# Performance work log

Measured on AMD Instinct MI355X. Metric: run time of the kernel, lower is better.

## Reference

```python
import jax, jax.numpy as jnp
import numpy as np

N, M, FEAT, POS, D, MSG, NCLS = 64, 32, 256, 6, 262, 128, 7


def setup_inputs() -> dict:
    key = jax.random.key(0)
    ks = jax.random.split(key, 12)
    s = 0.05
    p = lambda k, shape: jax.random.normal(k, shape, jnp.float32) * s
    return {
        "nodes_feature": jax.random.normal(ks[0], (N, M, FEAT), jnp.float32),
        "pos": jax.random.normal(ks[1], (N, M, POS), jnp.float32),
        "num_rec": jax.random.randint(ks[2], (N,), 1, M + 1),
        "link_w1": p(ks[3], (D, 2 * D)),
        "link_b1": jnp.zeros((D,), jnp.float32),
        "link_w2": p(ks[4], (D,)),
        "link_b2": jnp.zeros((), jnp.float32),
        "msg_w": p(ks[5], (MSG, D)),
        "msg_b": jnp.zeros((MSG,), jnp.float32),
        "gru_w_ih": p(ks[6], (3 * D, MSG)),
        "gru_w_hh": p(ks[7], (3 * D, D)),
        "gru_b_ih": jnp.zeros((3 * D,), jnp.float32),
        "gru_b_hh": jnp.zeros((3 * D,), jnp.float32),
        "ro_w1": p(ks[8], (MSG, D)),
        "ro_b1": jnp.zeros((MSG,), jnp.float32),
        "ro_w2": p(ks[9], (NCLS, MSG)),
        "ro_b2": jnp.zeros((NCLS,), jnp.float32),
    }


def reference(nodes_feature, pos, num_rec, link_w1, link_b1, link_w2, link_b2,
              msg_w, msg_b, gru_w_ih, gru_w_hh, gru_b_ih, gru_b_hh,
              ro_w1, ro_b1, ro_w2, ro_b2):
    # node_feat = [resnet_feat, pos]  -> (N, M, 262)
    nf = jnp.concatenate([nodes_feature, pos], axis=-1)
    n, m, d = nf.shape
    valid = jnp.arange(m)[None, :] < num_rec[:, None]          # (N, M)
    pair = valid[:, :, None] & valid[:, None, :]               # (N, M, M)

    # edge_feat[b,:,i,j] = concat(nf[b,i], nf[b,j]); zero for invalid pairs
    ef = jnp.concatenate([
        jnp.broadcast_to(nf[:, :, None, :], (n, m, m, d)),
        jnp.broadcast_to(nf[:, None, :, :], (n, m, m, d)),
    ], axis=-1) * pair[..., None].astype(nf.dtype)             # (N, M, M, 2D)

    # 1x1 convs == per-pair MLP
    hlink = jax.nn.relu(jnp.einsum('bnwc,dc->bnwd', ef, link_w1) + link_b1)
    attmat = jax.nn.sigmoid(jnp.einsum('bnwd,d->bnw', hlink, link_w2) + link_b2)

    # messages are only summed over valid sender nodes w
    att_m = attmat * valid[:, None, :].astype(attmat.dtype)    # (N, M, M)

    def gru_step(x, h):
        # PyTorch GRU cell: gates order (r, z, n)
        gx = x @ gru_w_ih.T + gru_b_ih
        gh = h @ gru_w_hh.T + gru_b_hh
        xr, xz, xn = jnp.split(gx, 3, axis=-1)
        hr, hz, hn = jnp.split(gh, 3, axis=-1)
        r = jax.nn.sigmoid(xr + hr)
        z = jax.nn.sigmoid(xz + hz)
        c = jnp.tanh(xn + r * hn)
        return (1.0 - z) * c + z * h

    vmask = valid[..., None].astype(nf.dtype)
    h_state = nf                                               # pass 0 input state
    for _ in range(2):                                         # two message-passing rounds
        msg = h_state @ msg_w.T + msg_b                        # (N, M, 128)
        m_v = jnp.einsum('bnw,bwk->bnk', att_m, msg)           # attention-weighted sum
        h_state = gru_step(m_v, h_state) * vmask               # invalid nodes stay zero

    pred = (jax.nn.relu(h_state @ ro_w1.T + ro_b1) @ ro_w2.T + ro_b2) * vmask
    return pred, attmat
```

## Files before the change

### kernel.cpp

```cpp
#include <hip/hip_runtime.h>
#include <math.h>

#define N_G   64
#define M_N   32
#define FEAT  256
#define POSD  6
#define D     262
#define MSG   128
#define NCLS  7

#define KA_S  424
#define KHW   288
#define KFULL 416
#define PSTR  320

#define S_PROJ (528*288)
#define S_MSG  (128*288)
#define S_RZ   (544*416)
#define S_XN   (272*128)
#define S_HN   (272*288)
#define S_RO   (128*288)
#define S_RO2  (16*128)

#define O_WPROJ 0u
#define O_WMSG  76032u
#define O_WRZ   94464u
#define O_WXN   207616u
#define O_WHN   225024u
#define O_WRO   264192u
#define O_WRO2  282624u
#define O_GB    283648u

typedef __attribute__((ext_vector_type(8))) short short8;
typedef __attribute__((ext_vector_type(4))) short short4v;
typedef __attribute__((ext_vector_type(4))) float floatx4;

#define MFMA __builtin_amdgcn_mfma_f32_16x16x32_bf16

__device__ __forceinline__ short f2bf(float f) {
    union { float f; unsigned u; } v; v.f = f;
    unsigned r = v.u + 0x7FFF + ((v.u >> 16) & 1);
    return (short)(r >> 16);
}
__device__ __forceinline__ float bf2f(short s) {
    union { float f; unsigned u; } v;
    v.u = ((unsigned)(unsigned short)s) << 16;
    return v.f;
}
__device__ __forceinline__ float sigf(float x) {
    return __builtin_amdgcn_rcpf(1.f + __expf(-x));
}
__device__ __forceinline__ float tanh_fast(float x) {
    float e = __expf(-2.f * fabsf(x));
    float t = (1.f - e) * __builtin_amdgcn_rcpf(1.f + e);
    return copysignf(t, x);
}

__global__ __launch_bounds__(256) void prep_kernel(
    const float* __restrict__ w1, const float* __restrict__ msg_w,
    const float* __restrict__ w_ih, const float* __restrict__ w_hh,
    const float* __restrict__ ro_w1, const float* __restrict__ ro_w2,
    const float* __restrict__ b_ih, const float* __restrict__ b_hh,
    float* __restrict__ ws)
{
    short* wproj = (short*)(ws + O_WPROJ);
    short* wmsg  = (short*)(ws + O_WMSG);
    short* wrz   = (short*)(ws + O_WRZ);
    short* wxn   = (short*)(ws + O_WXN);
    short* whn   = (short*)(ws + O_WHN);
    short* wro   = (short*)(ws + O_WRO);
    short* wro2  = (short*)(ws + O_WRO2);
    float* gb    = ws + O_GB;

    int row = blockIdx.x * 4 + (threadIdx.x >> 6);
    const int lane = threadIdx.x & 63;
    if (row >= 1892) return;

    if (row < 528) {
        const int n = row;
        short* out = wproj + n * 288;
        const float* src = (n < D) ? (w1 + n * 524) : (w1 + (n - D) * 524 + D);
        for (int k = lane; k < 288; k += 64) {
            float v = (k < D && n < 524) ? src[k] : 0.f;
            out[k] = f2bf(v);
        }
        return;
    }
    row -= 528;
    if (row < 128) {
        const int n = row;
        short* out = wmsg + n * 288;
        const float* src = msg_w + n * D;
        for (int k = lane; k < 288; k += 64)
            out[k] = f2bf(k < D ? src[k] : 0.f);
        return;
    }
    row -= 128;
    if (row < 544) {
        const int g = row;
        const int gi = (g < 272) ? 0 : 1;
        const int d = g - gi * 272;
        short* out = wrz + g * 416;
        if (d < D) {
            const int r = gi * D + d;
            const float* sih = w_ih + r * MSG;
            const float* shh = w_hh + r * D - 128;
            for (int k = lane; k < 416; k += 64) {
                float v;
                if (k < 128)            v = sih[k];
                else if (k < 128 + D)   v = shh[k];
                else                    v = 0.f;
                out[k] = f2bf(v);
            }
        } else {
            for (int k = lane; k < 416; k += 64) out[k] = 0;
        }
        return;
    }
    row -= 544;
    if (row < 272) {
        const int d = row;
        short* out = wxn + d * 128;
        const float* src = w_ih + (2 * D + d) * MSG;
        for (int k = lane; k < 128; k += 64)
            out[k] = f2bf(d < D ? src[k] : 0.f);
        return;
    }
    row -= 272;
    if (row < 272) {
        const int d = row;
        short* out = whn + d * 288;
        const float* src = w_hh + (2 * D + d) * D;
        for (int k = lane; k < 288; k += 64)
            out[k] = f2bf((d < D && k < D) ? src[k] : 0.f);
        return;
    }
    row -= 272;
    if (row < 128) {
        const int n = row;
        short* out = wro + n * 288;
        const float* src = ro_w1 + n * D;
        for (int k = lane; k < 288; k += 64)
            out[k] = f2bf(k < D ? src[k] : 0.f);
        return;
    }
    row -= 128;
    if (row < 16) {
        const int n = row;
        short* out = wro2 + n * 128;
        const float* src = ro_w2 + n * MSG;
        for (int k = lane; k < 128; k += 64)
            out[k] = f2bf(n < NCLS ? src[k] : 0.f);
        return;
    }
    row -= 16;
    {
        const int seg = row;
        float* out = gb + seg * 272;
        for (int d = lane; d < 272; d += 64) {
            float v = 0.f;
            if (d < D) {
                if (seg == 0)      v = b_ih[d] + b_hh[d];
                else if (seg == 1) v = b_ih[D + d] + b_hh[D + d];
                else if (seg == 2) v = b_ih[2 * D + d];
                else               v = b_hh[2 * D + d];
            }
            out[d] = v;
        }
    }
}

__global__ __launch_bounds__(512, 2) void fused_kernel(
    const float* __restrict__ nodes, const float* __restrict__ pos,
    const int* __restrict__ nrec_g,
    const float* __restrict__ b1g, const float* __restrict__ w2g,
    const float* __restrict__ b2g, const float* __restrict__ msg_bg,
    const float* __restrict__ ro_b1g, const float* __restrict__ ro_b2g,
    const float* __restrict__ ws,
    float* __restrict__ att_out, float* __restrict__ pred)
{
    const short* Wproj = (const short*)(ws + O_WPROJ);
    const short* Wmsg  = (const short*)(ws + O_WMSG);
    const short* Wrz   = (const short*)(ws + O_WRZ);
    const short* Wxn   = (const short*)(ws + O_WXN);
    const short* Whn   = (const short*)(ws + O_WHN);
    const short* Wro   = (const short*)(ws + O_WRO);
    const short* Wro2  = (const short*)(ws + O_WRO2);
    const float* gb    = ws + O_GB;

    __shared__ __align__(16) short bufA[32 * KA_S];
    __shared__ __align__(16) short bufB[32 * KA_S];
    __shared__ __align__(16) short paL[32 * PSTR];
    __shared__ __align__(16) short pbL[32 * PSTR];
    __shared__ __align__(16) short attL[32 * 40];
    __shared__ __align__(16) short msgT[128 * 40];
    __shared__ __align__(16) short hidL[32 * 136];
    __shared__ __align__(16) float b1L[PSTR], w2L[PSTR];

    const int b = blockIdx.x;
    const int tid = threadIdx.x;
    const int wave = tid >> 6, lane = tid & 63;
    const int quad = lane >> 4, lrow = lane & 15;

    floatx4 prm[10];
    {
        const floatx4* pb = (const floatx4*)(ws + O_WRZ);
        const int base = wave * 64 + lane;
#pragma unroll
        for (int p = 0; p < 10; ++p)
            prm[p] = pb[(p * 512 + base) * 8];
    }
    short8 wvA[9];
    {
        const short* bw = Wproj + (wave * 16 + lrow) * KHW + quad * 8;
#pragma unroll
        for (int kk = 0; kk < 9; ++kk) wvA[kk] = *(const short8*)(bw + kk * 32);
    }

    const int nr = nrec_g[b];

    for (int idx = tid; idx < 32 * 64; idx += 512) {
        int w = idx >> 6, c4 = idx & 63;
        floatx4 v = *(const floatx4*)(nodes + ((size_t)(b * 32 + w)) * FEAT + c4 * 4);
        short4v s; s[0] = f2bf(v[0]); s[1] = f2bf(v[1]); s[2] = f2bf(v[2]); s[3] = f2bf(v[3]);
        *(short4v*)(bufA + w * KA_S + 128 + c4 * 4) = s;
    }
    for (int idx = tid; idx < 32 * POSD; idx += 512) {
        int w = idx / POSD, c = idx % POSD;
        bufA[w * KA_S + 128 + FEAT + c] = f2bf(pos[((size_t)(b * 32 + w)) * POSD + c]);
    }
    for (int idx = tid; idx < 32 * 34; idx += 512) {
        int w = idx / 34, c = idx % 34;
        bufA[w * KA_S + 390 + c] = 0;
        bufB[w * KA_S + 390 + c] = 0;
    }
    for (int idx = tid; idx < 32 * (PSTR - D); idx += 512) {
        int w = idx / (PSTR - D), c = idx % (PSTR - D);
        paL[w * PSTR + D + c] = 0;
        pbL[w * PSTR + D + c] = 0;
    }
    for (int d = tid; d < PSTR; d += 512) {
        b1L[d] = (d < D) ? b1g[d] : 0.f;
        w2L[d] = (d < D) ? w2g[d] : 0.f;
    }
#pragma unroll
    for (int p = 0; p < 10; ++p) asm volatile("" :: "v"(prm[p]));
    __syncthreads();

    {
        auto store_proj = [&](int s, floatx4 acc0, floatx4 acc1) {
            int col = s * 16 + lrow;
#pragma unroll
            for (int rr = 0; rr < 4; ++rr) {
                int r0 = quad * 4 + rr;
                if (col < D) {
                    paL[r0 * PSTR + col] = f2bf(acc0[rr]);
                    paL[(r0 + 16) * PSTR + col] = f2bf(acc1[rr]);
                } else if (col < 2 * D) {
                    pbL[r0 * PSTR + (col - D)] = f2bf(acc0[rr]);
                    pbL[(r0 + 16) * PSTR + (col - D)] = f2bf(acc1[rr]);
                }
            }
        };
        auto store_msg = [&](int s, floatx4 acc0, floatx4 acc1) {
            int col = (s - 33) * 16 + lrow;
            float bias = msg_bg[col];
#pragma unroll
            for (int rr = 0; rr < 4; ++rr) {
                msgT[col * 40 + quad * 4 + rr] = f2bf(acc0[rr] + bias);
                msgT[col * 40 + 16 + quad * 4 + rr] = f2bf(acc1[rr] + bias);
            }
        };

        short8 aF0[9], aF1[9];
        {
            const short* ap = bufA + lrow * KA_S + 128 + quad * 8;
#pragma unroll
            for (int kk = 0; kk < 9; ++kk) {
                aF0[kk] = *(const short8*)(ap + kk * 32);
                aF1[kk] = *(const short8*)(ap + 16 * KA_S + kk * 32);
            }
        }
        short8 wvB[9];

#define P1_LOAD(DST, TT) do { \
            const short* bw_ = ((TT) < 33) \
                ? Wproj + ((TT) * 16 + lrow) * KHW + quad * 8 \
                : Wmsg + (((TT) - 33) * 16 + lrow) * KHW + quad * 8; \
            _Pragma("unroll") \
            for (int kk = 0; kk < 9; ++kk) DST[kk] = *(const short8*)(bw_ + kk * 32); \
        } while (0)

#define P1_TILE(W, TT) do { \
            floatx4 acc0_ = {}, acc1_ = {}; \
            _Pragma("unroll") \
            for (int kk = 0; kk < 9; ++kk) { \
                acc0_ = MFMA(aF0[kk], W[kk], acc0_, 0, 0, 0); \
                acc1_ = MFMA(aF1[kk], W[kk], acc1_, 0, 0, 0); \
            } \
            if ((TT) < 33) store_proj((TT), acc0_, acc1_); \
            else store_msg((TT), acc0_, acc1_); \
        } while (0)

        int t = wave;
        P1_LOAD(wvB, t + 8);
        P1_TILE(wvA, t);
        t += 8;
        P1_LOAD(wvA, t + 8);
        P1_TILE(wvB, t);
        t += 8;
        P1_LOAD(wvB, t + 8);
        P1_TILE(wvA, t);
        t += 8;
        P1_LOAD(wvA, t + 8);
        P1_TILE(wvB, t);
        t += 8;
        if (t + 8 < 41) P1_LOAD(wvB, t + 8);
        P1_TILE(wvA, t);
        t += 8;
        if (t < 41) P1_TILE(wvB, t);
#undef P1_LOAD
#undef P1_TILE
    }
    __syncthreads();

    {
        const int grp = tid >> 4;
        const int c16 = tid & 15;
        const float b2v = b2g[0];
        float pav[5][4], b1v[5][4], w2v[5][4];
#pragma unroll
        for (int k = 0; k < 5; ++k) {
            int dbase = c16 * 4 + 64 * k;
            short4v p = *(const short4v*)(paL + grp * PSTR + dbase);
            floatx4 bb = *(const floatx4*)(b1L + dbase);
            floatx4 ww = *(const floatx4*)(w2L + dbase);
#pragma unroll
            for (int e = 0; e < 4; ++e) {
                pav[k][e] = bf2f(p[e]); b1v[k][e] = bb[e]; w2v[k][e] = ww[e];
            }
        }
        float p0 = 0.f;
#pragma unroll
        for (int k = 0; k < 5; ++k)
#pragma unroll
            for (int e = 0; e < 4; ++e)
                p0 += fmaxf(b1v[k][e], 0.f) * w2v[k][e];
        p0 += __shfl_down(p0, 8, 16); p0 += __shfl_down(p0, 4, 16);
        p0 += __shfl_down(p0, 2, 16); p0 += __shfl_down(p0, 1, 16);
        float c0 = sigf(p0 + b2v);
        const bool vi = grp < nr;
        for (int j = 0; j < 32; ++j) {
            float a;
            if (j < nr && vi) {
                const short* pb = pbL + j * PSTR + c16 * 4;
                float s = 0.f;
#pragma unroll
                for (int k = 0; k < 5; ++k) {
                    short4v q = *(const short4v*)(pb + 64 * k);
#pragma unroll
                    for (int e = 0; e < 4; ++e) {
                        float v = pav[k][e] + bf2f(q[e]) + b1v[k][e];
                        s += fmaxf(v, 0.f) * w2v[k][e];
                    }
                }
                s += __shfl_down(s, 8, 16); s += __shfl_down(s, 4, 16);
                s += __shfl_down(s, 2, 16); s += __shfl_down(s, 1, 16);
                a = sigf(s + b2v);
            } else {
                a = c0;
            }
            if (c16 == 0) {
                att_out[((size_t)(b * 32 + grp)) * 32 + j] = a;
                attL[grp * 40 + j] = f2bf((j < nr) ? a : 0.f);
            }
        }
    }
    __syncthreads();

    for (int rnd = 0; rnd < 2; ++rnd) {
        short* src = rnd ? bufB : bufA;
        short* dst = rnd ? bufA : bufB;

        if (rnd) {
            int s = wave;
            const short* bw = Wmsg + (s * 16 + lrow) * KHW + quad * 8;
            short8 wm[9];
#pragma unroll
            for (int kk = 0; kk < 9; ++kk) wm[kk] = *(const short8*)(bw + kk * 32);
            floatx4 acc0 = {}, acc1 = {};
            const short* ap = src + lrow * KA_S + 128 + quad * 8;
#pragma unroll
            for (int kk = 0; kk < 9; ++kk) {
                short8 x0 = *(const short8*)(ap + kk * 32);
                short8 x1 = *(const short8*)(ap + 16 * KA_S + kk * 32);
                acc0 = MFMA(x0, wm[kk], acc0, 0, 0, 0);
                acc1 = MFMA(x1, wm[kk], acc1, 0, 0, 0);
            }
            int col = s * 16 + lrow;
            float bias = msg_bg[col];
#pragma unroll
            for (int rr = 0; rr < 4; ++rr) {
                msgT[col * 40 + quad * 4 + rr] = f2bf(acc0[rr] + bias);
                msgT[col * 40 + 16 + quad * 4 + rr] = f2bf(acc1[rr] + bias);
            }
            __syncthreads();
        }

        {
            int mi = wave & 1, ng = wave >> 1;
            short8 afrag = *(const short8*)(attL + (mi * 16 + lrow) * 40 + quad * 8);
            floatx4 acc0 = {}, acc1 = {};
            short8 bf0 = *(const short8*)(msgT + (ng * 32 + lrow) * 40 + quad * 8);
            short8 bf1 = *(const short8*)(msgT + (ng * 32 + 16 + lrow) * 40 + quad * 8);
            acc0 = MFMA(afrag, bf0, acc0, 0, 0, 0);
            acc1 = MFMA(afrag, bf1, acc1, 0, 0, 0);
#pragma unroll
            for (int rr = 0; rr < 4; ++rr) {
                int m = mi * 16 + quad * 4 + rr;
                src[m * KA_S + ng * 32 + lrow] = f2bf(acc0[rr]);
                src[m * KA_S + ng * 32 + 16 + lrow] = f2bf(acc1[rr]);
            }
        }
        __syncthreads();

        {
            short8 aA0[13], aA1[13];
            {
                const short* ap0 = src + lrow * KA_S + quad * 8;
#pragma unroll
                for (int kk = 0; kk < 13; ++kk) {
                    aA0[kk] = *(const short8*)(ap0 + kk * 32);
                    aA1[kk] = *(const short8*)(ap0 + 16 * KA_S + kk * 32);
                }
            }
            for (int s = wave; s < 17; s += 8) {
                const short* bpr = Wrz + (s * 16 + lrow) * KFULL + quad * 8;
                const short* bpz = bpr + 272 * KFULL;
                const short* bpx = Wxn + (s * 16 + lrow) * 128 + quad * 8;
                const short* bph = Whn + (s * 16 + lrow) * KHW + quad * 8;

                short8 wr[13];
#pragma unroll
                for (int kk = 0; kk < 13; ++kk) wr[kk] = *(const short8*)(bpr + kk * 32);

                floatx4 aR0 = {}, aR1 = {}, aZ0 = {}, aZ1 = {};
                floatx4 aN0 = {}, aN1 = {}, aH0 = {}, aH1 = {};
#pragma unroll
                for (int kk = 0; kk < 13; ++kk) {
                    aR0 = MFMA(aA0[kk], wr[kk], aR0, 0, 0, 0);
                    aR1 = MFMA(aA1[kk], wr[kk], aR1, 0, 0, 0);
                    if (kk < 4) {
                        short8 bx = *(const short8*)(bpx + kk * 32);
                        aN0 = MFMA(aA0[kk], bx, aN0, 0, 0, 0);
                        aN1 = MFMA(aA1[kk], bx, aN1, 0, 0, 0);
                    }
                    wr[kk] = *(const short8*)(bpz + kk * 32);
                }
#pragma unroll
                for (int kk = 0; kk < 13; ++kk) {
                    aZ0 = MFMA(aA0[kk], wr[kk], aZ0, 0, 0, 0);
                    aZ1 = MFMA(aA1[kk], wr[kk], aZ1, 0, 0, 0);
                    if (kk < 9) wr[kk] = *(const short8*)(bph + kk * 32);
                }
#pragma unroll
                for (int kk = 0; kk < 9; ++kk) {
                    aH0 = MFMA(aA0[kk + 4], wr[kk], aH0, 0, 0, 0);
                    aH1 = MFMA(aA1[kk + 4], wr[kk], aH1, 0, 0, 0);
                }

                int d = s * 16 + lrow;
                if (d < D) {
                    float bgr = gb[d], bgz = gb[272 + d];
                    float bxv = gb[544 + d], bhv = gb[816 + d];
#pragma unroll
                    for (int i = 0; i < 2; ++i) {
                        floatx4 vR = i ? aR1 : aR0, vZ = i ? aZ1 : aZ0;
                        floatx4 vN = i ? aN1 : aN0, vH = i ? aH1 : aH0;
#pragma unroll
                        for (int rr = 0; rr < 4; ++rr) {
                            int m = i * 16 + quad * 4 + rr;
                            float rg = sigf(vR[rr] + bgr);
                            float zg = sigf(vZ[rr] + bgz);
                            float cg = tanh_fast(vN[rr] + bxv + rg * (vH[rr] + bhv));
                            float hold = bf2f(src[m * KA_S + 128 + d]);
                            float hv = (1.f - zg) * cg + zg * hold;
                            if (m >= nr) hv = 0.f;
                            dst[m * KA_S + 128 + d] = f2bf(hv);
                        }
                    }
                }
            }
        }
        __syncthreads();
    }

    {
        int s = wave;
        const short* bw = Wro + (s * 16 + lrow) * KHW + quad * 8;
        short8 wv[9];
#pragma unroll
        for (int kk = 0; kk < 9; ++kk) wv[kk] = *(const short8*)(bw + kk * 32);
        floatx4 acc0 = {}, acc1 = {};
        const short* ap = bufA + lrow * KA_S + 128 + quad * 8;
#pragma unroll
        for (int kk = 0; kk < 9; ++kk) {
            short8 x0 = *(const short8*)(ap + kk * 32);
            short8 x1 = *(const short8*)(ap + 16 * KA_S + kk * 32);
            acc0 = MFMA(x0, wv[kk], acc0, 0, 0, 0);
            acc1 = MFMA(x1, wv[kk], acc1, 0, 0, 0);
        }
        int col = s * 16 + lrow;
        float bias = ro_b1g[col];
#pragma unroll
        for (int rr = 0; rr < 4; ++rr) {
            hidL[(quad * 4 + rr) * 136 + col] = f2bf(fmaxf(acc0[rr] + bias, 0.f));
            hidL[(16 + quad * 4 + rr) * 136 + col] = f2bf(fmaxf(acc1[rr] + bias, 0.f));
        }
    }
    __syncthreads();

    if (wave == 0) {
        const short* bw = Wro2 + lrow * 128 + quad * 8;
        short8 wv[4];
#pragma unroll
        for (int kk = 0; kk < 4; ++kk) wv[kk] = *(const short8*)(bw + kk * 32);
        floatx4 acc0 = {}, acc1 = {};
        const short* ap = hidL + lrow * 136 + quad * 8;
#pragma unroll
        for (int kk = 0; kk < 4; ++kk) {
            short8 x0 = *(const short8*)(ap + kk * 32);
            short8 x1 = *(const short8*)(ap + 16 * 136 + kk * 32);
            acc0 = MFMA(x0, wv[kk], acc0, 0, 0, 0);
            acc1 = MFMA(x1, wv[kk], acc1, 0, 0, 0);
        }
        int q = lrow;
        if (q < NCLS) {
            float bias = ro_b2g[q];
#pragma unroll
            for (int i = 0; i < 2; ++i) {
#pragma unroll
                for (int rr = 0; rr < 4; ++rr) {
                    int m = i * 16 + quad * 4 + rr;
                    float v = (i ? acc1[rr] : acc0[rr]) + bias;
                    if (m >= nr) v = 0.f;
                    pred[((size_t)(b * 32 + m)) * NCLS + q] = v;
                }
            }
        }
    }
}

extern "C" void kernel_launch(void* const* d_in, const int* in_sizes, int n_in,
                              void* d_out, int out_size, void* d_ws, size_t ws_size,
                              hipStream_t stream)
{
    const float* nodes = (const float*)d_in[0];
    const float* pos   = (const float*)d_in[1];
    const int*   nrec  = (const int*)d_in[2];
    const float* w1    = (const float*)d_in[3];
    const float* b1    = (const float*)d_in[4];
    const float* w2    = (const float*)d_in[5];
    const float* b2    = (const float*)d_in[6];
    const float* msg_w = (const float*)d_in[7];
    const float* msg_b = (const float*)d_in[8];
    const float* w_ih  = (const float*)d_in[9];
    const float* w_hh  = (const float*)d_in[10];
    const float* b_ih  = (const float*)d_in[11];
    const float* b_hh  = (const float*)d_in[12];
    const float* ro_w1 = (const float*)d_in[13];
    const float* ro_b1 = (const float*)d_in[14];
    const float* ro_w2 = (const float*)d_in[15];
    const float* ro_b2 = (const float*)d_in[16];
    float* ws   = (float*)d_ws;
    float* pred = (float*)d_out;
    float* attout = pred + (size_t)N_G * M_N * NCLS;

    prep_kernel<<<473, 256, 0, stream>>>(w1, msg_w, w_ih, w_hh, ro_w1, ro_w2,
                                         b_ih, b_hh, ws);
    fused_kernel<<<N_G, 512, 0, stream>>>(nodes, pos, nrec, b1, w2, b2, msg_b,
                                          ro_b1, ro_b2, ws, attout, pred);
}
```

Measured before the change: 150.3 us.

## Split fused per-graph kernel into multi-kernel pipeline with global-memory staging

Replaces the single 64-block fused kernel with a chain of smaller kernels (projection, attention, mixing, GRU per round, readout) that exchange intermediates through workspace buffers in global memory. Each stage is spread over many more blocks (e.g. 656, 256, 272 blocks) to fill more of the GPU's compute units than one block per graph. Input conversion to bf16 moves into the prep kernel. The cost is extra kernel launches and global-memory round trips in place of shared-memory reuse.

```diff
diff --git a/kernel.cpp b/kernel.cpp
--- a/kernel.cpp
+++ b/kernel.cpp
@@ -9,9 +9,9 @@
 #define MSG   128
 #define NCLS  7
 
-#define KA_S  424
 #define KHW   288
 #define KFULL 416
+#define HSTR  416
 #define PSTR  320
 
 #define S_PROJ (528*288)
@@ -30,6 +30,14 @@
 #define O_WRO   264192u
 #define O_WRO2  282624u
 #define O_GB    283648u
+#define O_GHA   284736u
+#define O_GHB   710720u
+#define O_GPA   1136704u
+#define O_GPB   1464384u
+#define O_GATT  1792064u
+#define O_GMSG  1833024u
+#define O_B1P   1996864u
+#define O_W2P   1997184u
 
 typedef __attribute__((ext_vector_type(8))) short short8;
 typedef __attribute__((ext_vector_type(4))) short short4v;
@@ -61,6 +69,8 @@
     const float* __restrict__ w_ih, const float* __restrict__ w_hh,
     const float* __restrict__ ro_w1, const float* __restrict__ ro_w2,
     const float* __restrict__ b_ih, const float* __restrict__ b_hh,
+    const float* __restrict__ b1g, const float* __restrict__ w2g,
+    const float* __restrict__ nodes, const float* __restrict__ pos,
     float* __restrict__ ws)
 {
     short* wproj = (short*)(ws + O_WPROJ);
@@ -74,23 +84,20 @@
 
     int row = blockIdx.x * 4 + (threadIdx.x >> 6);
     const int lane = threadIdx.x & 63;
-    if (row >= 1892) return;
+    if (row >= 5989) return;
 
     if (row < 528) {
         const int n = row;
         short* out = wproj + n * 288;
         const float* src = (n < D) ? (w1 + n * 524) : (w1 + (n - D) * 524 + D);
-        for (int k = lane; k < 288; k += 64) {
-            float v = (k < D && n < 524) ? src[k] : 0.f;
-            out[k] = f2bf(v);
-        }
+        for (int k = lane; k < 288; k += 64)
+            out[k] = f2bf((k < D && n < 524) ? src[k] : 0.f);
         return;
     }
     row -= 528;
     if (row < 128) {
-        const int n = row;
-        short* out = wmsg + n * 288;
-        const float* src = msg_w + n * D;
+        short* out = wmsg + row * 288;
+        const float* src = msg_w + row * D;
         for (int k = lane; k < 288; k += 64)
             out[k] = f2bf(k < D ? src[k] : 0.f);
         return;
@@ -137,24 +144,22 @@
     }
     row -= 272;
     if (row < 128) {
-        const int n = row;
-        short* out = wro + n * 288;
-        const float* src = ro_w1 + n * D;
+        short* out = wro + row * 288;
+        const float* src = ro_w1 + row * D;
         for (int k = lane; k < 288; k += 64)
             out[k] = f2bf(k < D ? src[k] : 0.f);
         return;
     }
     row -= 128;
     if (row < 16) {
-        const int n = row;
-        short* out = wro2 + n * 128;
-        const float* src = ro_w2 + n * MSG;
+        short* out = wro2 + row * 128;
+        const float* src = ro_w2 + row * MSG;
         for (int k = lane; k < 128; k += 64)
-            out[k] = f2bf(n < NCLS ? src[k] : 0.f);
+            out[k] = f2bf(row < NCLS ? src[k] : 0.f);
         return;
     }
     row -= 16;
-    {
+    if (row < 4) {
         const int seg = row;
         float* out = gb + seg * 272;
         for (int d = lane; d < 272; d += 64) {
@@ -167,348 +172,381 @@
             }
             out[d] = v;
         }
-    }
-}
-
-__global__ __launch_bounds__(512, 2) void fused_kernel(
-    const float* __restrict__ nodes, const float* __restrict__ pos,
-    const int* __restrict__ nrec_g,
-    const float* __restrict__ b1g, const float* __restrict__ w2g,
-    const float* __restrict__ b2g, const float* __restrict__ msg_bg,
-    const float* __restrict__ ro_b1g, const float* __restrict__ ro_b2g,
-    const float* __restrict__ ws,
-    float* __restrict__ att_out, float* __restrict__ pred)
-{
+        return;
+    }
+    row -= 4;
+    if (row < 1) {
+        float* b1p = ws + O_B1P;
+        float* w2p = ws + O_W2P;
+        for (int k = lane; k < 320; k += 64) {
+            b1p[k] = (k < D) ? b1g[k] : 0.f;
+            w2p[k] = (k < D) ? w2g[k] : 0.f;
+        }
+        return;
+    }
+    row -= 1;
+    if (row < 2048) {
+        const int b = row >> 5, w = row & 31;
+        short* out = (short*)(ws + O_GHA) + (size_t)(b * 32 + w) * HSTR + 128;
+        const float* nsrc = nodes + (size_t)(b * 32 + w) * FEAT;
+        const float* psrc = pos + (size_t)(b * 32 + w) * POSD;
+        for (int k = lane; k < 288; k += 64) {
+            float v = 0.f;
+            if (k < FEAT)             v = nsrc[k];
+            else if (k < FEAT + POSD) v = psrc[k - FEAT];
+            out[k] = f2bf(v);
+        }
+        return;
+    }
+    row -= 2048;
+    {
+        const int b = row >> 5, w = row & 31;
+        short* hb = (short*)(ws + O_GHB) + (size_t)(b * 32 + w) * HSTR + 128;
+        short* pa = (short*)(ws + O_GPA) + (size_t)(b * 32 + w) * PSTR;
+        short* pb = (short*)(ws + O_GPB) + (size_t)(b * 32 + w) * PSTR;
+        if (lane < 26) hb[D + lane] = 0;
+        if (lane < 58) { pa[D + lane] = 0; pb[D + lane] = 0; }
+    }
+}
+
+__global__ __launch_bounds__(256, 2) void k_proj(
+    const float* __restrict__ ws, const float* __restrict__ msg_bg)
+{
+    const short* GH   = (const short*)(ws + O_GHA);
+    short* GPA        = (short*)(ws + O_GPA);
+    short* GPB        = (short*)(ws + O_GPB);
+    short* GMSG       = (short*)(ws + O_GMSG);
     const short* Wproj = (const short*)(ws + O_WPROJ);
     const short* Wmsg  = (const short*)(ws + O_WMSG);
-    const short* Wrz   = (const short*)(ws + O_WRZ);
-    const short* Wxn   = (const short*)(ws + O_WXN);
-    const short* Whn   = (const short*)(ws + O_WHN);
-    const short* Wro   = (const short*)(ws + O_WRO);
-    const short* Wro2  = (const short*)(ws + O_WRO2);
-    const float* gb    = ws + O_GB;
-
-    __shared__ __align__(16) short bufA[32 * KA_S];
-    __shared__ __align__(16) short bufB[32 * KA_S];
-    __shared__ __align__(16) short paL[32 * PSTR];
-    __shared__ __align__(16) short pbL[32 * PSTR];
-    __shared__ __align__(16) short attL[32 * 40];
+
+    const int job = blockIdx.x * 4 + (threadIdx.x >> 6);
+    const int b = job / 41, t = job % 41;
+    const int lane = threadIdx.x & 63;
+    const int quad = lane >> 4, lrow = lane & 15;
+
+    const short* ap0 = GH + (size_t)(b * 32 + lrow) * HSTR + 128 + quad * 8;
+    const short* ap1 = ap0 + 16 * HSTR;
+    const short* bw = (t < 33)
+        ? Wproj + (t * 16 + lrow) * KHW + quad * 8
+        : Wmsg + ((t - 33) * 16 + lrow) * KHW + quad * 8;
+
+    short8 a0[9], a1[9], wv[9];
+#pragma unroll
+    for (int kk = 0; kk < 9; ++kk) {
+        a0[kk] = *(const short8*)(ap0 + kk * 32);
+        a1[kk] = *(const short8*)(ap1 + kk * 32);
+        wv[kk] = *(const short8*)(bw + kk * 32);
+    }
+    floatx4 acc0 = {}, acc1 = {};
+#pragma unroll
+    for (int kk = 0; kk < 9; ++kk) {
+        acc0 = MFMA(a0[kk], wv[kk], acc0, 0, 0, 0);
+        acc1 = MFMA(a1[kk], wv[kk], acc1, 0, 0, 0);
+    }
+    if (t < 33) {
+        int col = t * 16 + lrow;
+#pragma unroll
+        for (int rr = 0; rr < 4; ++rr) {
+            int r0 = quad * 4 + rr;
+            if (col < D) {
+                GPA[(size_t)(b * 32 + r0) * PSTR + col] = f2bf(acc0[rr]);
+                GPA[(size_t)(b * 32 + r0 + 16) * PSTR + col] = f2bf(acc1[rr]);
+            } else if (col < 2 * D) {
+                GPB[(size_t)(b * 32 + r0) * PSTR + (col - D)] = f2bf(acc0[rr]);
+                GPB[(size_t)(b * 32 + r0 + 16) * PSTR + (col - D)] = f2bf(acc1[rr]);
+            }
+        }
+    } else {
+        int col = (t - 33) * 16 + lrow;
+        float bias = msg_bg[col];
+#pragma unroll
+        for (int rr = 0; rr < 4; ++rr) {
+            GMSG[(size_t)b * 5120 + col * 40 + quad * 4 + rr] = f2bf(acc0[rr] + bias);
+            GMSG[(size_t)b * 5120 + col * 40 + 16 + quad * 4 + rr] = f2bf(acc1[rr] + bias);
+        }
+    }
+}
+
+__global__ __launch_bounds__(256, 4) void k_att(
+    const float* __restrict__ ws, const int* __restrict__ nrec_g,
+    const float* __restrict__ b2g, float* __restrict__ att_out)
+{
+    const short* GPA = (const short*)(ws + O_GPA);
+    const short* GPB = (const short*)(ws + O_GPB);
+    short* GATT      = (short*)(ws + O_GATT);
+    const float* b1p = ws + O_B1P;
+    const float* w2p = ws + O_W2P;
+
+    const int g = blockIdx.x * 16 + (threadIdx.x >> 4);
+    const int b = g >> 6;
+    const int rem = g & 63;
+    const int i = rem >> 1, jh = (rem & 1) * 16;
+    const int c16 = threadIdx.x & 15;
+    const int nr = nrec_g[b];
+    const float b2v = b2g[0];
+
+    float pav[5][4], b1v[5][4], w2v[5][4];
+#pragma unroll
+    for (int k = 0; k < 5; ++k) {
+        int dbase = c16 * 4 + 64 * k;
+        short4v p = *(const short4v*)(GPA + (size_t)(b * 32 + i) * PSTR + dbase);
+        floatx4 bb = *(const floatx4*)(b1p + dbase);
+        floatx4 ww = *(const floatx4*)(w2p + dbase);
+#pragma unroll
+        for (int e = 0; e < 4; ++e) {
+            pav[k][e] = bf2f(p[e]); b1v[k][e] = bb[e]; w2v[k][e] = ww[e];
+        }
+    }
+    float p0 = 0.f;
+#pragma unroll
+    for (int k = 0; k < 5; ++k)
+#pragma unroll
+        for (int e = 0; e < 4; ++e)
+            p0 += fmaxf(b1v[k][e], 0.f) * w2v[k][e];
+    p0 += __shfl_down(p0, 8, 16); p0 += __shfl_down(p0, 4, 16);
+    p0 += __shfl_down(p0, 2, 16); p0 += __shfl_down(p0, 1, 16);
+    float c0 = sigf(p0 + b2v);
+    const bool vi = i < nr;
+    for (int jj = 0; jj < 16; ++jj) {
+        int j = jh + jj;
+        float a;
+        if (j < nr && vi) {
+            const short* pb = GPB + (size_t)(b * 32 + j) * PSTR + c16 * 4;
+            float s = 0.f;
+#pragma unroll
+            for (int k = 0; k < 5; ++k) {
+                short4v q = *(const short4v*)(pb + 64 * k);
+#pragma unroll
+                for (int e = 0; e < 4; ++e) {
+                    float v = pav[k][e] + bf2f(q[e]) + b1v[k][e];
+                    s += fmaxf(v, 0.f) * w2v[k][e];
+                }
+            }
+            s += __shfl_down(s, 8, 16); s += __shfl_down(s, 4, 16);
+            s += __shfl_down(s, 2, 16); s += __shfl_down(s, 1, 16);
+            a = sigf(s + b2v);
+        } else {
+            a = c0;
+        }
+        if (c16 == 0) {
+            att_out[((size_t)(b * 32 + i)) * 32 + j] = a;
+            GATT[(size_t)b * 1280 + i * 40 + j] = f2bf((j < nr) ? a : 0.f);
+        }
+    }
+}
+
+__global__ __launch_bounds__(256, 4) void k_mix0(float* __restrict__ ws)
+{
+    const short* GATT = (const short*)(ws + O_GATT);
+    const short* GMSG = (const short*)(ws + O_GMSG);
+    short* GH         = (short*)(ws + O_GHA);
+
+    const int b = blockIdx.x;
+    const int tid = threadIdx.x;
+    const int ng = tid >> 6, lane = tid & 63;
+    const int quad = lane >> 4, lrow = lane & 15;
+
+    short8 af0 = *(const short8*)(GATT + (size_t)b * 1280 + lrow * 40 + quad * 8);
+    short8 af1 = *(const short8*)(GATT + (size_t)b * 1280 + (16 + lrow) * 40 + quad * 8);
+    short8 bf0 = *(const short8*)(GMSG + (size_t)b * 5120 + (ng * 32 + lrow) * 40 + quad * 8);
+    short8 bf1 = *(const short8*)(GMSG + (size_t)b * 5120 + (ng * 32 + 16 + lrow) * 40 + quad * 8);
+    floatx4 c00 = {}, c01 = {}, c10 = {}, c11 = {};
+    c00 = MFMA(af0, bf0, c00, 0, 0, 0);
+    c01 = MFMA(af0, bf1, c01, 0, 0, 0);
+    c10 = MFMA(af1, bf0, c10, 0, 0, 0);
+    c11 = MFMA(af1, bf1, c11, 0, 0, 0);
+#pragma unroll
+    for (int rr = 0; rr < 4; ++rr) {
+        int m0 = quad * 4 + rr;
+        GH[(size_t)(b * 32 + m0) * HSTR + ng * 32 + lrow] = f2bf(c00[rr]);
+        GH[(size_t)(b * 32 + m0) * HSTR + ng * 32 + 16 + lrow] = f2bf(c01[rr]);
+        GH[(size_t)(b * 32 + m0 + 16) * HSTR + ng * 32 + lrow] = f2bf(c10[rr]);
+        GH[(size_t)(b * 32 + m0 + 16) * HSTR + ng * 32 + 16 + lrow] = f2bf(c11[rr]);
+    }
+}
+
+__global__ __launch_bounds__(256, 2) void k_gru(
+    float* __restrict__ ws, const int* __restrict__ nrec_g, const int srcA)
+{
+    const short* src = (const short*)(ws + (srcA ? O_GHA : O_GHB));
+    short* dst       = (short*)(ws + (srcA ? O_GHB : O_GHA));
+    const short* Wrz = (const short*)(ws + O_WRZ);
+    const short* Wxn = (const short*)(ws + O_WXN);
+    const short* Whn = (const short*)(ws + O_WHN);
+    const float* gb  = ws + O_GB;
+
+    const int job = blockIdx.x * 4 + (threadIdx.x >> 6);
+    const int b = job / 17, s = job % 17;
+    const int nr = nrec_g[b];
+    const int lane = threadIdx.x & 63;
+    const int quad = lane >> 4, lrow = lane & 15;
+
+    const short* ap0 = src + (size_t)(b * 32 + lrow) * HSTR + quad * 8;
+    const short* ap1 = ap0 + 16 * HSTR;
+    short8 aA0[13], aA1[13];
+#pragma unroll
+    for (int kk = 0; kk < 13; ++kk) {
+        aA0[kk] = *(const short8*)(ap0 + kk * 32);
+        aA1[kk] = *(const short8*)(ap1 + kk * 32);
+    }
+    const short* bpr = Wrz + (s * 16 + lrow) * KFULL + quad * 8;
+    const short* bpz = bpr + 272 * KFULL;
+    const short* bpx = Wxn + (s * 16 + lrow) * 128 + quad * 8;
+    const short* bph = Whn + (s * 16 + lrow) * KHW + quad * 8;
+
+    short8 wr[13];
+#pragma unroll
+    for (int kk = 0; kk < 13; ++kk) wr[kk] = *(const short8*)(bpr + kk * 32);
+
+    floatx4 aR0 = {}, aR1 = {}, aZ0 = {}, aZ1 = {};
+    floatx4 aN0 = {}, aN1 = {}, aH0 = {}, aH1 = {};
+#pragma unroll
+    for (int kk = 0; kk < 13; ++kk) {
+        aR0 = MFMA(aA0[kk], wr[kk], aR0, 0, 0, 0);
+        aR1 = MFMA(aA1[kk], wr[kk], aR1, 0, 0, 0);
+        if (kk < 4) {
+            short8 bx = *(const short8*)(bpx + kk * 32);
+            aN0 = MFMA(aA0[kk], bx, aN0, 0, 0, 0);
+            aN1 = MFMA(aA1[kk], bx, aN1, 0, 0, 0);
+        }
+        wr[kk] = *(const short8*)(bpz + kk * 32);
+    }
+#pragma unroll
+    for (int kk = 0; kk < 13; ++kk) {
+        aZ0 = MFMA(aA0[kk], wr[kk], aZ0, 0, 0, 0);
+        aZ1 = MFMA(aA1[kk], wr[kk], aZ1, 0, 0, 0);
+        if (kk < 9) wr[kk] = *(const short8*)(bph + kk * 32);
+    }
+#pragma unroll
+    for (int kk = 0; kk < 9; ++kk) {
+        aH0 = MFMA(aA0[kk + 4], wr[kk], aH0, 0, 0, 0);
+        aH1 = MFMA(aA1[kk + 4], wr[kk], aH1, 0, 0, 0);
+    }
+
+    const int d = s * 16 + lrow;
+    if (d < D) {
+        float bgr = gb[d], bgz = gb[272 + d];
+        float bxv = gb[544 + d], bhv = gb[816 + d];
+#pragma unroll
+        for (int i = 0; i < 2; ++i) {
+            floatx4 vR = i ? aR1 : aR0, vZ = i ? aZ1 : aZ0;
+            floatx4 vN = i ? aN1 : aN0, vH = i ? aH1 : aH0;
+#pragma unroll
+            for (int rr = 0; rr < 4; ++rr) {
+                int m = i * 16 + quad * 4 + rr;
+                float rg = sigf(vR[rr] + bgr);
+                float zg = sigf(vZ[rr] + bgz);
+                float cg = tanh_fast(vN[rr] + bxv + rg * (vH[rr] + bhv));
+                float hold = bf2f(src[(size_t)(b * 32 + m) * HSTR + 128 + d]);
+                float hv = (1.f - zg) * cg + zg * hold;
+                if (m >= nr) hv = 0.f;
+                dst[(size_t)(b * 32 + m) * HSTR + 128 + d] = f2bf(hv);
+            }
+        }
+    }
+}
+
+__global__ __launch_bounds__(256, 2) void k_msgmix1(
+    float* __restrict__ ws, const float* __restrict__ msg_bg)
+{
     __shared__ __align__(16) short msgT[128 * 40];
-    __shared__ __align__(16) short hidL[32 * 136];
-    __shared__ __align__(16) float b1L[PSTR], w2L[PSTR];
+    short* GHB        = (short*)(ws + O_GHB);
+    const short* GATT = (const short*)(ws + O_GATT);
+    const short* Wmsg = (const short*)(ws + O_WMSG);
 
     const int b = blockIdx.x;
     const int tid = threadIdx.x;
     const int wave = tid >> 6, lane = tid & 63;
     const int quad = lane >> 4, lrow = lane & 15;
 
-    floatx4 prm[10];
+    const short* ap0 = GHB + (size_t)(b * 32 + lrow) * HSTR + 128 + quad * 8;
+    const short* ap1 = ap0 + 16 * HSTR;
+    short8 a0[9], a1[9];
+#pragma unroll
+    for (int kk = 0; kk < 9; ++kk) {
+        a0[kk] = *(const short8*)(ap0 + kk * 32);
+        a1[kk] = *(const short8*)(ap1 + kk * 32);
+    }
+#pragma unroll
+    for (int ti = 0; ti < 2; ++ti) {
+        int s = wave + ti * 4;
+        const short* bw = Wmsg + (s * 16 + lrow) * KHW + quad * 8;
+        short8 wv[9];
+#pragma unroll
+        for (int kk = 0; kk < 9; ++kk) wv[kk] = *(const short8*)(bw + kk * 32);
+        floatx4 acc0 = {}, acc1 = {};
+#pragma unroll
+        for (int kk = 0; kk < 9; ++kk) {
+            acc0 = MFMA(a0[kk], wv[kk], acc0, 0, 0, 0);
+            acc1 = MFMA(a1[kk], wv[kk], acc1, 0, 0, 0);
+        }
+        int col = s * 16 + lrow;
+        float bias = msg_bg[col];
+#pragma unroll
+        for (int rr = 0; rr < 4; ++rr) {
+            msgT[col * 40 + quad * 4 + rr] = f2bf(acc0[rr] + bias);
+            msgT[col * 40 + 16 + quad * 4 + rr] = f2bf(acc1[rr] + bias);
+        }
+    }
+    __syncthreads();
     {
-        const floatx4* pb = (const floatx4*)(ws + O_WRZ);
-        const int base = wave * 64 + lane;
-#pragma unroll
-        for (int p = 0; p < 10; ++p)
-            prm[p] = pb[(p * 512 + base) * 8];
-    }
-    short8 wvA[9];
-    {
-        const short* bw = Wproj + (wave * 16 + lrow) * KHW + quad * 8;
-#pragma unroll
-        for (int kk = 0; kk < 9; ++kk) wvA[kk] = *(const short8*)(bw + kk * 32);
-    }
-
+        const int ng = wave;
+        short8 af0 = *(const short8*)(GATT + (size_t)b * 1280 + lrow * 40 + quad * 8);
+        short8 af1 = *(const short8*)(GATT + (size_t)b * 1280 + (16 + lrow) * 40 + quad * 8);
+        short8 bf0 = *(const short8*)(msgT + (ng * 32 + lrow) * 40 + quad * 8);
+        short8 bf1 = *(const short8*)(msgT + (ng * 32 + 16 + lrow) * 40 + quad * 8);
+        floatx4 c00 = {}, c01 = {}, c10 = {}, c11 = {};
+        c00 = MFMA(af0, bf0, c00, 0, 0, 0);
+        c01 = MFMA(af0, bf1, c01, 0, 0, 0);
+        c10 = MFMA(af1, bf0, c10, 0, 0, 0);
+        c11 = MFMA(af1, bf1, c11, 0, 0, 0);
+#pragma unroll
+        for (int rr = 0; rr < 4; ++rr) {
+            int m0 = quad * 4 + rr;
+            GHB[(size_t)(b * 32 + m0) * HSTR + ng * 32 + lrow] = f2bf(c00[rr]);
+            GHB[(size_t)(b * 32 + m0) * HSTR + ng * 32 + 16 + lrow] = f2bf(c01[rr]);
+            GHB[(size_t)(b * 32 + m0 + 16) * HSTR + ng * 32 + lrow] = f2bf(c10[rr]);
+            GHB[(size_t)(b * 32 + m0 + 16) * HSTR + ng * 32 + 16 + lrow] = f2bf(c11[rr]);
+        }
+    }
+}
+
+__global__ __launch_bounds__(256, 2) void k_out(
+    const float* __restrict__ ws, const int* __restrict__ nrec_g,
+    const float* __restrict__ ro_b1g, const float* __restrict__ ro_b2g,
+    float* __restrict__ pred)
+{
+    __shared__ __align__(16) short hidL[32 * 136];
+    const short* GHA  = (const short*)(ws + O_GHA);
+    const short* Wro  = (const short*)(ws + O_WRO);
+    const short* Wro2 = (const short*)(ws + O_WRO2);
+
+    const int b = blockIdx.x;
+    const int tid = threadIdx.x;
+    const int wave = tid >> 6, lane = tid & 63;
+    const int quad = lane >> 4, lrow = lane & 15;
     const int nr = nrec_g[b];
 
-    for (int idx = tid; idx < 32 * 64; idx += 512) {
-        int w = idx >> 6, c4 = idx & 63;
-        floatx4 v = *(const floatx4*)(nodes + ((size_t)(b * 32 + w)) * FEAT + c4 * 4);
-        short4v s; s[0] = f2bf(v[0]); s[1] = f2bf(v[1]); s[2] = f2bf(v[2]); s[3] = f2bf(v[3]);
-        *(short4v*)(bufA + w * KA_S + 128 + c4 * 4) = s;
-    }
-    for (int idx = tid; idx < 32 * POSD; idx += 512) {
-        int w = idx / POSD, c = idx % POSD;
-        bufA[w * KA_S + 128 + FEAT + c] = f2bf(pos[((size_t)(b * 32 + w)) * POSD + c]);
-    }
-    for (int idx = tid; idx < 32 * 34; idx += 512) {
-        int w = idx / 34, c = idx % 34;
-        bufA[w * KA_S + 390 + c] = 0;
-        bufB[w * KA_S + 390 + c] = 0;
-    }
-    for (int idx = tid; idx < 32 * (PSTR - D); idx += 512) {
-        int w = idx / (PSTR - D), c = idx % (PSTR - D);
-        paL[w * PSTR + D + c] = 0;
-        pbL[w * PSTR + D + c] = 0;
-    }
-    for (int d = tid; d < PSTR; d += 512) {
-        b1L[d] = (d < D) ? b1g[d] : 0.f;
-        w2L[d] = (d < D) ? w2g[d] : 0.f;
-    }
-#pragma unroll
-    for (int p = 0; p < 10; ++p) asm volatile("" :: "v"(prm[p]));
-    __syncthreads();
-
-    {
-        auto store_proj = [&](int s, floatx4 acc0, floatx4 acc1) {
-            int col = s * 16 + lrow;
-#pragma unroll
-            for (int rr = 0; rr < 4; ++rr) {
-                int r0 = quad * 4 + rr;
-                if (col < D) {
-                    paL[r0 * PSTR + col] = f2bf(acc0[rr]);
-                    paL[(r0 + 16) * PSTR + col] = f2bf(acc1[rr]);
-                } else if (col < 2 * D) {
-                    pbL[r0 * PSTR + (col - D)] = f2bf(acc0[rr]);
-                    pbL[(r0 + 16) * PSTR + (col - D)] = f2bf(acc1[rr]);
-                }
-            }
-        };
-        auto store_msg = [&](int s, floatx4 acc0, floatx4 acc1) {
-            int col = (s - 33) * 16 + lrow;
-            float bias = msg_bg[col];
-#pragma unroll
-            for (int rr = 0; rr < 4; ++rr) {
-                msgT[col * 40 + quad * 4 + rr] = f2bf(acc0[rr] + bias);
-                msgT[col * 40 + 16 + quad * 4 + rr] = f2bf(acc1[rr] + bias);
-            }
-        };
-
-        short8 aF0[9], aF1[9];
-        {
-            const short* ap = bufA + lrow * KA_S + 128 + quad * 8;
-#pragma unroll
-            for (int kk = 0; kk < 9; ++kk) {
-                aF0[kk] = *(const short8*)(ap + kk * 32);
-                aF1[kk] = *(const short8*)(ap + 16 * KA_S + kk * 32);
-            }
-        }
-        short8 wvB[9];
-
-#define P1_LOAD(DST, TT) do { \
-            const short* bw_ = ((TT) < 33) \
-                ? Wproj + ((TT) * 16 + lrow) * KHW + quad * 8 \
-                : Wmsg + (((TT) - 33) * 16 + lrow) * KHW + quad * 8; \
-            _Pragma("unroll") \
-            for (int kk = 0; kk < 9; ++kk) DST[kk] = *(const short8*)(bw_ + kk * 32); \
-        } while (0)
-
-#define P1_TILE(W, TT) do { \
-            floatx4 acc0_ = {}, acc1_ = {}; \
-            _Pragma("unroll") \
-            for (int kk = 0; kk < 9; ++kk) { \
-                acc0_ = MFMA(aF0[kk], W[kk], acc0_, 0, 0, 0); \
-                acc1_ = MFMA(aF1[kk], W[kk], acc1_, 0, 0, 0); \
-            } \
-            if ((TT) < 33) store_proj((TT), acc0_, acc1_); \
-            else store_msg((TT), acc0_, acc1_); \
-        } while (0)
-
-        int t = wave;
-        P1_LOAD(wvB, t + 8);
-        P1_TILE(wvA, t);
-        t += 8;
-        P1_LOAD(wvA, t + 8);
-        P1_TILE(wvB, t);
-        t += 8;
-        P1_LOAD(wvB, t + 8);
-        P1_TILE(wvA, t);
-        t += 8;
-        P1_LOAD(wvA, t + 8);
-        P1_TILE(wvB, t);
-        t += 8;
-        if (t + 8 < 41) P1_LOAD(wvB, t + 8);
-        P1_TILE(wvA, t);
-        t += 8;
-        if (t < 41) P1_TILE(wvB, t);
-#undef P1_LOAD
-#undef P1_TILE
-    }
-    __syncthreads();
-
-    {
-        const int grp = tid >> 4;
-        const int c16 = tid & 15;
-        const float b2v = b2g[0];
-        float pav[5][4], b1v[5][4], w2v[5][4];
-#pragma unroll
-        for (int k = 0; k < 5; ++k) {
-            int dbase = c16 * 4 + 64 * k;
-            short4v p = *(const short4v*)(paL + grp * PSTR + dbase);
-            floatx4 bb = *(const floatx4*)(b1L + dbase);
-            floatx4 ww = *(const floatx4*)(w2L + dbase);
-#pragma unroll
-            for (int e = 0; e < 4; ++e) {
-                pav[k][e] = bf2f(p[e]); b1v[k][e] = bb[e]; w2v[k][e] = ww[e];
-            }
-        }
-        float p0 = 0.f;
-#pragma unroll
-        for (int k = 0; k < 5; ++k)
-#pragma unroll
-            for (int e = 0; e < 4; ++e)
-                p0 += fmaxf(b1v[k][e], 0.f) * w2v[k][e];
-        p0 += __shfl_down(p0, 8, 16); p0 += __shfl_down(p0, 4, 16);
-        p0 += __shfl_down(p0, 2, 16); p0 += __shfl_down(p0, 1, 16);
-        float c0 = sigf(p0 + b2v);
-        const bool vi = grp < nr;
-        for (int j = 0; j < 32; ++j) {
-            float a;
-            if (j < nr && vi) {
-                const short* pb = pbL + j * PSTR + c16 * 4;
-                float s = 0.f;
-#pragma unroll
-                for (int k = 0; k < 5; ++k) {
-                    short4v q = *(const short4v*)(pb + 64 * k);
-#pragma unroll
-                    for (int e = 0; e < 4; ++e) {
-                        float v = pav[k][e] + bf2f(q[e]) + b1v[k][e];
-                        s += fmaxf(v, 0.f) * w2v[k][e];
-                    }
-                }
-                s += __shfl_down(s, 8, 16); s += __shfl_down(s, 4, 16);
-                s += __shfl_down(s, 2, 16); s += __shfl_down(s, 1, 16);
-                a = sigf(s + b2v);
-            } else {
-                a = c0;
-            }
-            if (c16 == 0) {
-                att_out[((size_t)(b * 32 + grp)) * 32 + j] = a;
-                attL[grp * 40 + j] = f2bf((j < nr) ? a : 0.f);
-            }
-        }
-    }
-    __syncthreads();
-
-    for (int rnd = 0; rnd < 2; ++rnd) {
-        short* src = rnd ? bufB : bufA;
-        short* dst = rnd ? bufA : bufB;
-
-        if (rnd) {
-            int s = wave;
-            const short* bw = Wmsg + (s * 16 + lrow) * KHW + quad * 8;
-            short8 wm[9];
-#pragma unroll
-            for (int kk = 0; kk < 9; ++kk) wm[kk] = *(const short8*)(bw + kk * 32);
-            floatx4 acc0 = {}, acc1 = {};
-            const short* ap = src + lrow * KA_S + 128 + quad * 8;
-#pragma unroll
-            for (int kk = 0; kk < 9; ++kk) {
-                short8 x0 = *(const short8*)(ap + kk * 32);
-                short8 x1 = *(const short8*)(ap + 16 * KA_S + kk * 32);
-                acc0 = MFMA(x0, wm[kk], acc0, 0, 0, 0);
-                acc1 = MFMA(x1, wm[kk], acc1, 0, 0, 0);
-            }
-            int col = s * 16 + lrow;
-            float bias = msg_bg[col];
-#pragma unroll
-            for (int rr = 0; rr < 4; ++rr) {
-                msgT[col * 40 + quad * 4 + rr] = f2bf(acc0[rr] + bias);
-                msgT[col * 40 + 16 + quad * 4 + rr] = f2bf(acc1[rr] + bias);
-            }
-            __syncthreads();
-        }
-
-        {
-            int mi = wave & 1, ng = wave >> 1;
-            short8 afrag = *(const short8*)(attL + (mi * 16 + lrow) * 40 + quad * 8);
-            floatx4 acc0 = {}, acc1 = {};
-            short8 bf0 = *(const short8*)(msgT + (ng * 32 + lrow) * 40 + quad * 8);
-            short8 bf1 = *(const short8*)(msgT + (ng * 32 + 16 + lrow) * 40 + quad * 8);
-            acc0 = MFMA(afrag, bf0, acc0, 0, 0, 0);
-            acc1 = MFMA(afrag, bf1, acc1, 0, 0, 0);
-#pragma unroll
-            for (int rr = 0; rr < 4; ++rr) {
-                int m = mi * 16 + quad * 4 + rr;
-                src[m * KA_S + ng * 32 + lrow] = f2bf(acc0[rr]);
-                src[m * KA_S + ng * 32 + 16 + lrow] = f2bf(acc1[rr]);
-            }
-        }
-        __syncthreads();
-
-        {
-            short8 aA0[13], aA1[13];
-            {
-                const short* ap0 = src + lrow * KA_S + quad * 8;
-#pragma unroll
-                for (int kk = 0; kk < 13; ++kk) {
-                    aA0[kk] = *(const short8*)(ap0 + kk * 32);
-                    aA1[kk] = *(const short8*)(ap0 + 16 * KA_S + kk * 32);
-                }
-            }
-            for (int s = wave; s < 17; s += 8) {
-                const short* bpr = Wrz + (s * 16 + lrow) * KFULL + quad * 8;
-                const short* bpz = bpr + 272 * KFULL;
-                const short* bpx = Wxn + (s * 16 + lrow) * 128 + quad * 8;
-                const short* bph = Whn + (s * 16 + lrow) * KHW + quad * 8;
-
-                short8 wr[13];
-#pragma unroll
-                for (int kk = 0; kk < 13; ++kk) wr[kk] = *(const short8*)(bpr + kk * 32);
-
-                floatx4 aR0 = {}, aR1 = {}, aZ0 = {}, aZ1 = {};
-                floatx4 aN0 = {}, aN1 = {}, aH0 = {}, aH1 = {};
-#pragma unroll
-                for (int kk = 0; kk < 13; ++kk) {
-                    aR0 = MFMA(aA0[kk], wr[kk], aR0, 0, 0, 0);
-                    aR1 = MFMA(aA1[kk], wr[kk], aR1, 0, 0, 0);
-                    if (kk < 4) {
-                        short8 bx = *(const short8*)(bpx + kk * 32);
-                        aN0 = MFMA(aA0[kk], bx, aN0, 0, 0, 0);
-                        aN1 = MFMA(aA1[kk], bx, aN1, 0, 0, 0);
-                    }
-                    wr[kk] = *(const short8*)(bpz + kk * 32);
-                }
-#pragma unroll
-                for (int kk = 0; kk < 13; ++kk) {
-                    aZ0 = MFMA(aA0[kk], wr[kk], aZ0, 0, 0, 0);
-                    aZ1 = MFMA(aA1[kk], wr[kk], aZ1, 0, 0, 0);
-                    if (kk < 9) wr[kk] = *(const short8*)(bph + kk * 32);
-                }
-#pragma unroll
-                for (int kk = 0; kk < 9; ++kk) {
-                    aH0 = MFMA(aA0[kk + 4], wr[kk], aH0, 0, 0, 0);
-                    aH1 = MFMA(aA1[kk + 4], wr[kk], aH1, 0, 0, 0);
-                }
-
-                int d = s * 16 + lrow;
-                if (d < D) {
-                    float bgr = gb[d], bgz = gb[272 + d];
-                    float bxv = gb[544 + d], bhv = gb[816 + d];
-#pragma unroll
-                    for (int i = 0; i < 2; ++i) {
-                        floatx4 vR = i ? aR1 : aR0, vZ = i ? aZ1 : aZ0;
-                        floatx4 vN = i ? aN1 : aN0, vH = i ? aH1 : aH0;
-#pragma unroll
-                        for (int rr = 0; rr < 4; ++rr) {
-                            int m = i * 16 + quad * 4 + rr;
-                            float rg = sigf(vR[rr] + bgr);
-                            float zg = sigf(vZ[rr] + bgz);
-                            float cg = tanh_fast(vN[rr] + bxv + rg * (vH[rr] + bhv));
-                            float hold = bf2f(src[m * KA_S + 128 + d]);
-                            float hv = (1.f - zg) * cg + zg * hold;
-                            if (m >= nr) hv = 0.f;
-                            dst[m * KA_S + 128 + d] = f2bf(hv);
-                        }
-                    }
-                }
-            }
-        }
-        __syncthreads();
-    }
-
-    {
-        int s = wave;
+    const short* ap0 = GHA + (size_t)(b * 32 + lrow) * HSTR + 128 + quad * 8;
+    const short* ap1 = ap0 + 16 * HSTR;
+    short8 a0[9], a1[9];
+#pragma unroll
+    for (int kk = 0; kk < 9; ++kk) {
+        a0[kk] = *(const short8*)(ap0 + kk * 32);
+        a1[kk] = *(const short8*)(ap1 + kk * 32);
+    }
+#pragma unroll
+    for (int ti = 0; ti < 2; ++ti) {
+        int s = wave + ti * 4;
         const short* bw = Wro + (s * 16 + lrow) * KHW + quad * 8;
         short8 wv[9];
 #pragma unroll
         for (int kk = 0; kk < 9; ++kk) wv[kk] = *(const short8*)(bw + kk * 32);
         floatx4 acc0 = {}, acc1 = {};
-        const short* ap = bufA + lrow * KA_S + 128 + quad * 8;
 #pragma unroll
         for (int kk = 0; kk < 9; ++kk) {
-            short8 x0 = *(const short8*)(ap + kk * 32);
-            short8 x1 = *(const short8*)(ap + 16 * KA_S + kk * 32);
-            acc0 = MFMA(x0, wv[kk], acc0, 0, 0, 0);
-            acc1 = MFMA(x1, wv[kk], acc1, 0, 0, 0);
+            acc0 = MFMA(a0[kk], wv[kk], acc0, 0, 0, 0);
+            acc1 = MFMA(a1[kk], wv[kk], acc1, 0, 0, 0);
         }
         int col = s * 16 + lrow;
         float bias = ro_b1g[col];
@@ -519,7 +557,6 @@
         }
     }
     __syncthreads();
-
     if (wave == 0) {
         const short* bw = Wro2 + lrow * 128 + quad * 8;
         short8 wv[4];
@@ -576,8 +613,13 @@
     float* pred = (float*)d_out;
     float* attout = pred + (size_t)N_G * M_N * NCLS;
 
-    prep_kernel<<<473, 256, 0, stream>>>(w1, msg_w, w_ih, w_hh, ro_w1, ro_w2,
-                                         b_ih, b_hh, ws);
-    fused_kernel<<<N_G, 512, 0, stream>>>(nodes, pos, nrec, b1, w2, b2, msg_b,
-                                          ro_b1, ro_b2, ws, attout, pred);
-}
+    prep_kernel<<<1498, 256, 0, stream>>>(w1, msg_w, w_ih, w_hh, ro_w1, ro_w2,
+                                          b_ih, b_hh, b1, w2, nodes, pos, ws);
+    k_proj<<<656, 256, 0, stream>>>(ws, msg_b);
+    k_att<<<256, 256, 0, stream>>>(ws, nrec, b2, attout);
+    k_mix0<<<64, 256, 0, stream>>>(ws);
+    k_gru<<<272, 256, 0, stream>>>(ws, nrec, 1);
+    k_msgmix1<<<64, 256, 0, stream>>>(ws, msg_b);
+    k_gru<<<272, 256, 0, stream>>>(ws, nrec, 0);
+    k_out<<<64, 256, 0, stream>>>(ws, nrec, ro_b1, ro_b2, pred);
+}
```

After: 150.7 us. No clear change (+0.2%).
